# Optimization experiments

Measured on AMD Instinct MI355X. Metric: run time of the kernel, lower is better.

## Reference

```python
import jax, jax.numpy as jnp
import numpy as np

B, L, D, H = 2, 2048, 512, 8
DH = D // H
THRESHOLD = 0.1


def setup_inputs() -> dict:
    key = jax.random.key(0)
    ks = jax.random.split(key, 8)
    s = 0.02  # weight scale to keep activations sane
    return {
        "q_x": jax.random.normal(ks[0], (B, L, D), jnp.float32),
        "k_x": jax.random.normal(ks[1], (B, L, D), jnp.float32),
        "v_x": jax.random.normal(ks[2], (B, L, D), jnp.float32),
        "energy_coeffs": jax.random.normal(ks[3], (B, L, 16), jnp.float32),
        "Wq": jax.random.normal(ks[4], (D, D), jnp.float32) * s,
        "bq": jnp.zeros((D,), jnp.float32),
        "Wk": jax.random.normal(ks[5], (D, D), jnp.float32) * s,
        "bk": jnp.zeros((D,), jnp.float32),
        "Wv": jax.random.normal(ks[6], (D, D), jnp.float32) * s,
        "bv": jnp.zeros((D,), jnp.float32),
        "Wo": jax.random.normal(ks[7], (D, D), jnp.float32) * s,
        "bo": jnp.zeros((D,), jnp.float32),
    }


def reference(q_x, k_x, v_x, energy_coeffs, Wq, bq, Wk, bk, Wv, bv, Wo, bo):
    b, l, d = q_x.shape
    # QKV projections (torch Linear: x @ W.T + b), split heads -> [B,H,L,Dh]
    Q = (q_x @ Wq.T + bq).reshape(b, l, H, DH).transpose(0, 2, 1, 3)
    K = (k_x @ Wk.T + bk).reshape(b, -1, H, DH).transpose(0, 2, 1, 3)
    V = (v_x @ Wv.T + bv).reshape(b, -1, H, DH).transpose(0, 2, 1, 3)
    scores = jnp.einsum("bhqd,bhkd->bhqk", Q, K) / jnp.sqrt(jnp.float32(DH))
    # straight-through energy-based key mask
    energy = jnp.abs(energy_coeffs).mean(axis=-1)  # [B, Lk]
    soft = jax.nn.sigmoid((energy - THRESHOLD) * 10.0)
    hard = (energy > THRESHOLD).astype(q_x.dtype)
    mask_val = soft + jax.lax.stop_gradient(hard - soft)  # fwd=hard, grad=soft
    scores = scores + (1.0 - mask_val)[:, None, None, :] * (-1e9)
    attn = jax.nn.softmax(scores, axis=-1)
    out = jnp.einsum("bhqk,bhkd->bhqd", attn, V)
    out = out.transpose(0, 2, 1, 3).reshape(b, l, d)
    return out @ Wo.T + bo
```

## Files before the change

### kernel.cpp

```cpp
#include <hip/hip_runtime.h>
#include <stdint.h>

#define B_ 2
#define L_ 2048
#define D_ 512
#define H_ 8
#define DH_ 64

using frag8 = __attribute__((ext_vector_type(8))) short;
using bf4   = __attribute__((ext_vector_type(4))) short;
using f32x4 = __attribute__((ext_vector_type(4))) float;
using u32x4 = __attribute__((ext_vector_type(4))) unsigned int;

#define QSC 0.18033688011112042f

__device__ __forceinline__ unsigned short f2bf(float f) {
    unsigned int u = __float_as_uint(f);
    u += 0x7fffu + ((u >> 16) & 1u);
    return (unsigned short)(u >> 16);
}

__device__ __forceinline__ unsigned int cvtpk(float lo, float hi_) {
    unsigned int r;
    asm("v_cvt_pk_bf16_f32 %0, %1, %2" : "=v"(r) : "v"(lo), "v"(hi_));
    return r;
}

__device__ __forceinline__ void gl2lds16(const void* g, void* lds) {
    __builtin_amdgcn_global_load_lds((const __attribute__((address_space(1))) void*)g,
                                     (__attribute__((address_space(3))) void*)lds,
                                     16, 0, 0);
}

__global__ __launch_bounds__(256) void cvt_mask_kernel(
    const float* __restrict__ qx, const float* __restrict__ kx, const float* __restrict__ vx,
    const float* __restrict__ Wq, const float* __restrict__ Wk, const float* __restrict__ Wv,
    const float* __restrict__ Wo, const float* __restrict__ ec,
    unsigned short* qb, unsigned short* kb, unsigned short* vb,
    unsigned short* wqb, unsigned short* wkb, unsigned short* wvb, unsigned short* wob,
    float* __restrict__ mk)
{
    const long NA = (long)B_ * L_ * D_;
    const long NW = (long)D_ * D_;
    const long total4 = (3 * NA + 4 * NW) / 4;
    long q4 = (long)blockIdx.x * 256 + threadIdx.x;
    if (q4 < total4) {
        long i = q4 * 4;
        const float* src; unsigned short* dst; long off;
        if (i < NA)            { src = qx; dst = qb; off = i; }
        else if (i < 2 * NA)   { src = kx; dst = kb; off = i - NA; }
        else if (i < 3 * NA)   { src = vx; dst = vb; off = i - 2 * NA; }
        else {
            long j = i - 3 * NA;
            int w = (int)(j / NW);
            off = j - (long)w * NW;
            src = (w == 0) ? Wq : (w == 1) ? Wk : (w == 2) ? Wv : Wo;
            dst = (w == 0) ? wqb : (w == 1) ? wkb : (w == 2) ? wvb : wob;
        }
        float4 v = *(const float4*)(src + off);
        ushort4 o;
        o.x = f2bf(v.x); o.y = f2bf(v.y); o.z = f2bf(v.z); o.w = f2bf(v.w);
        *(ushort4*)(dst + off) = o;
    } else {
        long i = q4 - total4;
        if (i < B_ * L_) {
            const float4* p4 = (const float4*)(ec + i * 16);
            float s = 0.0f;
#pragma unroll
            for (int j = 0; j < 4; ++j) {
                float4 v = p4[j];
                s += fabsf(v.x) + fabsf(v.y) + fabsf(v.z) + fabsf(v.w);
            }
            float energy = s * (1.0f / 16.0f);
            mk[i] = (energy > 0.1f) ? 0.0f : -1.0e9f;
        }
    }
}

struct GemmArgs { const unsigned short* A; const unsigned short* W;
                  const float* bias; void* C; int mode; };

template<int BM, int BN>
__global__ __launch_bounds__(256) void gemm_kernel(GemmArgs a0, GemmArgs a1, GemmArgs a2,
                                                   int M, int N, int K)
{
    const int nwg = gridDim.x * gridDim.y * gridDim.z;
    int flat = blockIdx.x + gridDim.x * (blockIdx.y + gridDim.y * blockIdx.z);
    int swz  = (flat & 7) * (nwg >> 3) + (flat >> 3);
    const int bx = swz % gridDim.x;
    int t2 = swz / gridDim.x;
    const int by = t2 % gridDim.y;
    const int bz = t2 / gridDim.y;

    GemmArgs ga = bz == 0 ? a0 : (bz == 1 ? a1 : a2);
    const unsigned short* __restrict__ A = ga.A;
    const unsigned short* __restrict__ W = ga.W;
    const float* __restrict__ bias = ga.bias;

    constexpr int MF = BM / 32;
    constexpr int NF = BN / 32;

    __shared__ __align__(16) unsigned short As[2][BM * 64];
    __shared__ __align__(16) unsigned short Bs[2][BN * 64];

    const int tid  = threadIdx.x;
    const int lane = tid & 63;
    const int wave = tid >> 6;
    const int hi   = lane >> 4;
    const int ln   = lane & 15;
    const int wr   = wave >> 1;
    const int wc   = wave & 1;

    const long mBase = (long)by * BM;
    const long nBase = (long)bx * BN;

    f32x4 acc[MF][NF];
#pragma unroll
    for (int m = 0; m < MF; ++m)
#pragma unroll
        for (int n = 0; n < NF; ++n) acc[m][n] = (f32x4){0.f, 0.f, 0.f, 0.f};

#define GSTAGE(KT, BUF) do {                                                    \
    _Pragma("unroll")                                                           \
    for (int i_ = 0; i_ < BM / 32; ++i_) {                                      \
        int cl_ = i_ * 256 + tid;                                               \
        int r_ = cl_ >> 3, c_ = cl_ & 7, s_ = c_ ^ (r_ & 7);                    \
        gl2lds16(A + (mBase + r_) * K + (KT) + s_ * 8, As[BUF] + cl_ * 8);      \
    }                                                                           \
    _Pragma("unroll")                                                           \
    for (int i_ = 0; i_ < BN / 32; ++i_) {                                      \
        int cl_ = i_ * 256 + tid;                                               \
        int r_ = cl_ >> 3, c_ = cl_ & 7, s_ = c_ ^ (r_ & 7);                    \
        gl2lds16(W + (nBase + r_) * K + (KT) + s_ * 8, Bs[BUF] + cl_ * 8);      \
    }                                                                           \
} while (0)

    GSTAGE(0, 0);
    __syncthreads();

    const int nk = K / 64;
    for (int t = 0; t < nk; ++t) {
        const int buf = t & 1;
        if (t + 1 < nk) GSTAGE((t + 1) * 64, buf ^ 1);

        frag8 af[2][MF], bfr[2][NF];
#pragma unroll
        for (int kk = 0; kk < 2; ++kk) {
#pragma unroll
            for (int m = 0; m < MF; ++m) {
                int row = wr * (BM / 2) + m * 16 + ln;
                int c = (kk * 4 + hi) ^ (row & 7);
                af[kk][m] = *(const frag8*)(As[buf] + row * 64 + c * 8);
            }
#pragma unroll
            for (int n = 0; n < NF; ++n) {
                int row = wc * (BN / 2) + n * 16 + ln;
                int c = (kk * 4 + hi) ^ (row & 7);
                bfr[kk][n] = *(const frag8*)(Bs[buf] + row * 64 + c * 8);
            }
        }
        __builtin_amdgcn_s_setprio(1);
#pragma unroll
        for (int kk = 0; kk < 2; ++kk)
#pragma unroll
            for (int m = 0; m < MF; ++m)
#pragma unroll
                for (int n = 0; n < NF; ++n)
                    acc[m][n] = __builtin_amdgcn_mfma_f32_16x16x32_bf16(af[kk][m], bfr[kk][n], acc[m][n], 0, 0, 0);
        __builtin_amdgcn_s_setprio(0);
        __syncthreads();
    }
#undef GSTAGE

    const int mode = ga.mode;
#pragma unroll
    for (int m = 0; m < MF; ++m) {
#pragma unroll
        for (int n = 0; n < NF; ++n) {
            long col = nBase + wc * (BN / 2) + n * 16 + ln;
            float bv = bias[col];
#pragma unroll
            for (int j = 0; j < 4; ++j) {
                long row = mBase + wr * (BM / 2) + m * 16 + hi * 4 + j;
                float v = acc[m][n][j] + bv;
                if (mode == 3) {
                    ((float*)ga.C)[row * N + col] = v;
                } else if (mode == 2) {
                    int dh = (int)col & 63;
                    int swv = ((dh & 7) << 1) | ((dh >> 3) & 1);
                    long nt = (row & ~63L) | (long)(((((int)(row >> 2)) & 15) ^ swv) << 2) | (row & 3);
                    ((unsigned short*)ga.C)[col * (long)(B_ * L_) + nt] = f2bf(v);
                } else {
                    if (mode == 1) v *= QSC;
                    ((unsigned short*)ga.C)[row * N + col] = f2bf(v);
                }
            }
        }
    }
}

__global__ __launch_bounds__(512, 4) void attn_kernel(
    const unsigned short* __restrict__ Qg, const unsigned short* __restrict__ Kg,
    const unsigned short* __restrict__ Vt, const float* __restrict__ mkg,
    unsigned short* __restrict__ Og)
{
    const int tid  = threadIdx.x;
    const int lane = tid & 63;
    const int wave = tid >> 6;
    const int grp  = wave >> 2;
    const int wq   = wave & 3;
    const int gtid = tid & 255;
    const int hi   = lane >> 4;
    const int ln   = lane & 15;

    const int bh = blockIdx.y;
    const int b  = bh >> 3, h = bh & 7;
    const unsigned short* Qb = Qg + ((long)b * L_) * D_ + h * DH_;
    const unsigned short* Kb = Kg + ((long)b * L_) * D_ + h * DH_;
    const unsigned short* Vb = Vt + (long)(h * DH_) * (B_ * L_) + (long)b * L_;
    const float* mkb = mkg + (long)b * L_;

    __shared__ __align__(16) char smem[65536];
    unsigned short* KsG = (unsigned short*)(smem + grp * 32768);
    unsigned short* VsG = (unsigned short*)(smem + grp * 32768 + 16384);

    const int q0 = blockIdx.x * 64 + wq * 16;

    frag8 qf[2];
#pragma unroll
    for (int ks = 0; ks < 2; ++ks)
        qf[ks] = *(const frag8*)(Qb + (long)(q0 + ln) * D_ + ks * 32 + hi * 8);

    const int sw  = ((ln & 7) << 1) | ((ln >> 3) & 1);
    const int sl0 = ((hi     ) ^ sw) << 2;
    const int sl1 = ((hi + 4 ) ^ sw) << 2;
    const int sl2 = ((hi + 8 ) ^ sw) << 2;
    const int sl3 = ((hi + 12) ^ sw) << 2;

#define STAGE(TT, BUF) do {                                                     \
    _Pragma("unroll")                                                           \
    for (int c2_ = 0; c2_ < 2; ++c2_) {                                         \
        int cl_ = c2_ * 256 + gtid;                                             \
        int r_ = cl_ >> 3, c_ = cl_ & 7;                                        \
        gl2lds16(Kb + (long)((TT) * 64 + r_) * D_ + ((c_ ^ (r_ & 7)) << 3),     \
                 KsG + (BUF) * 4096 + cl_ * 8);                                 \
        gl2lds16(Vb + (long)r_ * (B_ * L_) + (TT) * 64 + (c_ << 3),             \
                 VsG + (BUF) * 4096 + cl_ * 8);                                 \
    }                                                                           \
} while (0)

    STAGE(grp, 0);
    __syncthreads();

    f32x4 o[4];
#pragma unroll
    for (int g = 0; g < 4; ++g) o[g] = (f32x4){0.f, 0.f, 0.f, 0.f};
    float m_run = -__builtin_inff();
    float l_run = 0.0f;

    for (int i = 0; i < 16; ++i) {
        const int T = 2 * i + grp;
        const int buf = i & 1;

        float4 m40 = *(const float4*)(mkb + T * 64 +      4 * hi);
        float4 m41 = *(const float4*)(mkb + T * 64 + 16 + 4 * hi);
        float4 m42 = *(const float4*)(mkb + T * 64 + 32 + 4 * hi);
        float4 m43 = *(const float4*)(mkb + T * 64 + 48 + 4 * hi);

        if (i < 15) STAGE(2 * (i + 1) + grp, buf ^ 1);

        const unsigned short* Kl = KsG + buf * 4096;
        const unsigned short* Vl = VsG + buf * 4096;

        f32x4 sv[4];
#pragma unroll
        for (int sh = 0; sh < 4; ++sh) sv[sh] = (f32x4){0.f, 0.f, 0.f, 0.f};
        __builtin_amdgcn_s_setprio(1);
#pragma unroll
        for (int sh = 0; sh < 4; ++sh) {
            int key = sh * 16 + ln;
#pragma unroll
            for (int ks = 0; ks < 2; ++ks) {
                frag8 kf = *(const frag8*)(Kl + key * 64 + (((ks * 4 + hi) ^ (ln & 7)) << 3));
                sv[sh] = __builtin_amdgcn_mfma_f32_16x16x32_bf16(kf, qf[ks], sv[sh], 0, 0, 0);
            }
        }
        __builtin_amdgcn_s_setprio(0);

        float sc[16];
        sc[0]  = sv[0][0] + m40.x; sc[1]  = sv[0][1] + m40.y;
        sc[2]  = sv[0][2] + m40.z; sc[3]  = sv[0][3] + m40.w;
        sc[4]  = sv[1][0] + m41.x; sc[5]  = sv[1][1] + m41.y;
        sc[6]  = sv[1][2] + m41.z; sc[7]  = sv[1][3] + m41.w;
        sc[8]  = sv[2][0] + m42.x; sc[9]  = sv[2][1] + m42.y;
        sc[10] = sv[2][2] + m42.z; sc[11] = sv[2][3] + m42.w;
        sc[12] = sv[3][0] + m43.x; sc[13] = sv[3][1] + m43.y;
        sc[14] = sv[3][2] + m43.z; sc[15] = sv[3][3] + m43.w;

        float t0 = fmaxf(fmaxf(sc[0], sc[1]), sc[2]);
        float t1 = fmaxf(fmaxf(sc[3], sc[4]), sc[5]);
        float t2 = fmaxf(fmaxf(sc[6], sc[7]), sc[8]);
        float t3 = fmaxf(fmaxf(sc[9], sc[10]), sc[11]);
        float t4 = fmaxf(fmaxf(sc[12], sc[13]), sc[14]);
        float tmax = fmaxf(fmaxf(fmaxf(t0, t1), fmaxf(t2, t3)), fmaxf(t4, sc[15]));
        tmax = fmaxf(tmax, __shfl_xor(tmax, 16));
        tmax = fmaxf(tmax, __shfl_xor(tmax, 32));

        if (!__all(tmax <= m_run)) {
            float m_new = fmaxf(m_run, tmax);
            float alpha = __builtin_amdgcn_exp2f(m_run - m_new);
            float a0 = __shfl(alpha, 4 * hi + 0);
            float a1 = __shfl(alpha, 4 * hi + 1);
            float a2 = __shfl(alpha, 4 * hi + 2);
            float a3 = __shfl(alpha, 4 * hi + 3);
#pragma unroll
            for (int g = 0; g < 4; ++g) {
                o[g][0] *= a0; o[g][1] *= a1; o[g][2] *= a2; o[g][3] *= a3;
            }
            l_run *= alpha;
            m_run = m_new;
        }

        float p[16];
#pragma unroll
        for (int j = 0; j < 16; ++j) p[j] = __builtin_amdgcn_exp2f(sc[j] - m_run);
        float s01 = (p[0] + p[1]) + (p[2] + p[3]);
        float s23 = (p[4] + p[5]) + (p[6] + p[7]);
        float s45 = (p[8] + p[9]) + (p[10] + p[11]);
        float s67 = (p[12] + p[13]) + (p[14] + p[15]);
        float ps = (s01 + s23) + (s45 + s67);
        ps += __shfl_xor(ps, 16);
        ps += __shfl_xor(ps, 32);
        l_run += ps;

        union PU { u32x4 u; frag8 f; } p0u, p1u;
        p0u.u = (u32x4){cvtpk(p[0], p[1]),  cvtpk(p[2], p[3]),
                        cvtpk(p[4], p[5]),  cvtpk(p[6], p[7])};
        p1u.u = (u32x4){cvtpk(p[8], p[9]),  cvtpk(p[10], p[11]),
                        cvtpk(p[12], p[13]), cvtpk(p[14], p[15])};

        __builtin_amdgcn_s_setprio(1);
#pragma unroll
        for (int g = 0; g < 4; ++g) {
            int rowb = (g * 16 + ln) * 64;
            bf4 a0 = *(const bf4*)(Vl + rowb + sl0);
            bf4 a1 = *(const bf4*)(Vl + rowb + sl1);
            bf4 a2 = *(const bf4*)(Vl + rowb + sl2);
            bf4 a3 = *(const bf4*)(Vl + rowb + sl3);
            frag8 vf0 = __builtin_shufflevector(a0, a1, 0, 1, 2, 3, 4, 5, 6, 7);
            frag8 vf1 = __builtin_shufflevector(a2, a3, 0, 1, 2, 3, 4, 5, 6, 7);
            o[g] = __builtin_amdgcn_mfma_f32_16x16x32_bf16(p0u.f, vf0, o[g], 0, 0, 0);
            o[g] = __builtin_amdgcn_mfma_f32_16x16x32_bf16(p1u.f, vf1, o[g], 0, 0, 0);
        }
        __builtin_amdgcn_s_setprio(0);

        __syncthreads();
    }
#undef STAGE

    float* oX = (float*)smem;
    float* mX = (float*)(smem + 64 * 68 * 4);
    float* lX = mX + 64;

    if (grp == 1) {
#pragma unroll
        for (int g = 0; g < 4; ++g)
#pragma unroll
            for (int j = 0; j < 4; ++j)
                oX[(wq * 16 + 4 * hi + j) * 68 + g * 16 + ln] = o[g][j];
        if (hi == 0) { mX[wq * 16 + ln] = m_run; lX[wq * 16 + ln] = l_run; }
    }
    __syncthreads();
    if (grp == 0) {
#pragma unroll
        for (int j = 0; j < 4; ++j) {
            int q = 4 * hi + j;
            float mA = __shfl(m_run, q);
            float lA = __shfl(l_run, q);
            float mB = mX[wq * 16 + q];
            float lB = lX[wq * 16 + q];
            float mm = fmaxf(mA, mB);
            float aA = __builtin_amdgcn_exp2f(mA - mm);
            float aB = __builtin_amdgcn_exp2f(mB - mm);
            float inv = 1.0f / (lA * aA + lB * aB);
            aA *= inv; aB *= inv;
#pragma unroll
            for (int g = 0; g < 4; ++g) {
                float v = o[g][j] * aA + oX[(wq * 16 + q) * 68 + g * 16 + ln] * aB;
                long idx = ((long)b * L_ + q0 + q) * D_ + h * DH_ + g * 16 + ln;
                Og[idx] = f2bf(v);
            }
        }
    }
}

extern "C" void kernel_launch(void* const* d_in, const int* in_sizes, int n_in,
                              void* d_out, int out_size, void* d_ws, size_t ws_size,
                              hipStream_t stream)
{
    const float* qx = (const float*)d_in[0];
    const float* kx = (const float*)d_in[1];
    const float* vx = (const float*)d_in[2];
    const float* ec = (const float*)d_in[3];
    const float* Wq = (const float*)d_in[4];
    const float* bq = (const float*)d_in[5];
    const float* Wk = (const float*)d_in[6];
    const float* bk = (const float*)d_in[7];
    const float* Wv = (const float*)d_in[8];
    const float* bv = (const float*)d_in[9];
    const float* Wo = (const float*)d_in[10];
    const float* bo = (const float*)d_in[11];
    float* out = (float*)d_out;

    const long NA = (long)B_ * L_ * D_;
    const long NW = (long)D_ * D_;

    unsigned short* qb  = (unsigned short*)d_ws;
    unsigned short* kb  = qb + NA;
    unsigned short* vb  = kb + NA;
    unsigned short* wqb = vb + NA;
    unsigned short* wkb = wqb + NW;
    unsigned short* wvb = wkb + NW;
    unsigned short* wob = wvb + NW;
    unsigned short* Qp  = wob + NW;
    unsigned short* Kp  = Qp + NA;
    unsigned short* Vtp = Kp + NA;
    unsigned short* Ap  = qb;
    float*          mk  = (float*)(Vtp + NA);

    const long total4 = (3 * NA + 4 * NW) / 4;
    const long nblk = (total4 + B_ * L_ + 255) / 256;
    cvt_mask_kernel<<<dim3((unsigned)nblk), dim3(256), 0, stream>>>(
        qx, kx, vx, Wq, Wk, Wv, Wo, ec, qb, kb, vb, wqb, wkb, wvb, wob, mk);

    GemmArgs zq = {qb, wqb, bq, Qp, 1};
    GemmArgs zk = {kb, wkb, bk, Kp, 0};
    GemmArgs zv = {vb, wvb, bv, Vtp, 2};
    gemm_kernel<64, 128><<<dim3(4, 64, 3), dim3(256), 0, stream>>>(zq, zk, zv, B_ * L_, D_, D_);

    attn_kernel<<<dim3(L_ / 64, B_ * H_), dim3(512), 0, stream>>>(Qp, Kp, Vtp, mk, Ap);

    GemmArgs zo = {Ap, wob, bo, out, 3};
    gemm_kernel<64, 64><<<dim3(8, 64, 1), dim3(256), 0, stream>>>(zo, zo, zo, B_ * L_, D_, D_);
}
```

Before: 78.56 us.

## Replace syncthreads with partial vmcnt waits to overlap next-tile loads

In both the GEMM and attention kernels, the full __syncthreads after issuing async global-to-LDS loads is replaced by an s_waitcnt vmcnt(N) that waits only for the previous stage's loads, followed by a raw s_barrier. This lets the prefetch of the next tile stay in flight while the current tile is computed, instead of draining every outstanding load at each barrier. The hand-counted vmcnt values (NL, 8, 4) must match the exact number of loads issued, including the mask float4 loads in attention. A miscount would race on LDS data.

```diff
diff --git a/kernel.cpp b/kernel.cpp
--- a/kernel.cpp
+++ b/kernel.cpp
@@ -30,6 +30,11 @@
     __builtin_amdgcn_global_load_lds((const __attribute__((address_space(1))) void*)g,
                                      (__attribute__((address_space(3))) void*)lds,
                                      16, 0, 0);
+}
+
+template<int N>
+__device__ __forceinline__ void vmwait() {
+    asm volatile("s_waitcnt vmcnt(%0)" :: "n"(N) : "memory");
 }
 
 __global__ __launch_bounds__(256) void cvt_mask_kernel(
@@ -99,6 +104,7 @@
 
     constexpr int MF = BM / 32;
     constexpr int NF = BN / 32;
+    constexpr int NL = BM / 32 + BN / 32;
 
     __shared__ __align__(16) unsigned short As[2][BM * 64];
     __shared__ __align__(16) unsigned short Bs[2][BN * 64];
@@ -136,12 +142,18 @@
 } while (0)
 
     GSTAGE(0, 0);
-    __syncthreads();
 
     const int nk = K / 64;
     for (int t = 0; t < nk; ++t) {
         const int buf = t & 1;
-        if (t + 1 < nk) GSTAGE((t + 1) * 64, buf ^ 1);
+        if (t + 1 < nk) {
+            GSTAGE((t + 1) * 64, buf ^ 1);
+            vmwait<NL>();
+        } else {
+            vmwait<0>();
+        }
+        __builtin_amdgcn_s_barrier();
+        __builtin_amdgcn_sched_barrier(0);
 
         frag8 af[2][MF], bfr[2][NF];
 #pragma unroll
@@ -168,7 +180,8 @@
                 for (int n = 0; n < NF; ++n)
                     acc[m][n] = __builtin_amdgcn_mfma_f32_16x16x32_bf16(af[kk][m], bfr[kk][n], acc[m][n], 0, 0, 0);
         __builtin_amdgcn_s_setprio(0);
-        __syncthreads();
+        __builtin_amdgcn_sched_barrier(0);
+        __builtin_amdgcn_s_barrier();
     }
 #undef GSTAGE
 
@@ -250,7 +263,6 @@
 } while (0)
 
     STAGE(grp, 0);
-    __syncthreads();
 
     f32x4 o[4];
 #pragma unroll
@@ -266,8 +278,16 @@
         float4 m41 = *(const float4*)(mkb + T * 64 + 16 + 4 * hi);
         float4 m42 = *(const float4*)(mkb + T * 64 + 32 + 4 * hi);
         float4 m43 = *(const float4*)(mkb + T * 64 + 48 + 4 * hi);
-
-        if (i < 15) STAGE(2 * (i + 1) + grp, buf ^ 1);
+        __builtin_amdgcn_sched_barrier(0);
+
+        if (i < 15) {
+            STAGE(2 * (i + 1) + grp, buf ^ 1);
+            vmwait<8>();
+        } else {
+            vmwait<4>();
+        }
+        __builtin_amdgcn_s_barrier();
+        __builtin_amdgcn_sched_barrier(0);
 
         const unsigned short* Kl = KsG + buf * 4096;
         const unsigned short* Vl = VsG + buf * 4096;
@@ -354,7 +374,8 @@
         }
         __builtin_amdgcn_s_setprio(0);
 
-        __syncthreads();
+        __builtin_amdgcn_sched_barrier(0);
+        __builtin_amdgcn_s_barrier();
     }
 #undef STAGE
 
```

After: 79.43 us. No clear change (+1.1%).
